# Kernel optimization log

Hardware: AMD Instinct MI355X
Metric: run time of the kernel (lower is better)

Reference implementation:

```python
import jax, jax.numpy as jnp
import numpy as np

K = 100  # sliding-window size hard-coded in the original forward


def setup_inputs() -> dict:
    key = jax.random.key(0)
    x = jax.random.normal(key, (32, 1, 1124, 1124), dtype=jnp.float32)
    return {"x": x}


def reference(x):
    # Sliding 100x100 mean over every stride-1 patch (gq == patch mean),
    # computed via a 2D integral image (summed-area table) so we never
    # materialize the [B, C, outH, outW, K, K] patch tensor.
    B, C, H, W = x.shape
    s = jnp.cumsum(jnp.cumsum(x, axis=2), axis=3)
    # pad one zero row/col at the front -> S has shape [B, C, H+1, W+1]
    S = jnp.pad(s, ((0, 0), (0, 0), (1, 0), (1, 0)))
    sums = (S[:, :, K:, K:] - S[:, :, :-K, K:]
            - S[:, :, K:, :-K] + S[:, :, :-K, :-K])  # [B, C, H-K+1, W-K+1]
    # gq averages over the whole patch (all channels + spatial) -> 1 channel out
    out = jnp.sum(sums, axis=1, keepdims=True) / jnp.asarray(K * K * C, x.dtype)
    return out  # [B, 1, H-99, W-99]
```

## Files before the change

kernel.cpp:

```cpp
#include <hip/hip_runtime.h>


#define H_IN    1124
#define W_IN    1124
#define KWIN    100
#define W_OUT   1025
#define H_OUT   1025
#define TSTR    1032
#define NBANDS  13
#define BANDR   79

typedef float    f32x4 __attribute__((ext_vector_type(4)));
typedef _Float16 f16x4 __attribute__((ext_vector_type(4)));

struct alignas(8) h4 { _Float16 a, b, c, d; };

__global__ __launch_bounds__(256) void hslide_kernel(
    const float* __restrict__ x,
    _Float16* __restrict__ T)
{
    __shared__ float srow[W_IN];
    __shared__ float ps[284];
    __shared__ float qs[280];

    const int row = blockIdx.x;
    const int tid = threadIdx.x;
    const f32x4* xr4 = (const f32x4*)(x + (size_t)row * W_IN);

    for (int i = tid; i < 281; i += 256)
        ((f32x4*)srow)[i] = __builtin_nontemporal_load(xr4 + i);
    __syncthreads();

    f32x4 lo = ((const f32x4*)srow)[tid];
    const float myps = lo[0] + lo[1] + lo[2] + lo[3];
    ps[tid] = myps;
    float myps2 = 0.f;
    if (tid < 25) {
        f32x4 v = ((const f32x4*)srow)[256 + tid];
        myps2 = v[0] + v[1] + v[2] + v[3];
        ps[256 + tid] = myps2;
    }
    __syncthreads();

    qs[tid] = myps + ps[tid + 1] + ps[tid + 2] + ps[tid + 3];
    if (tid < 22)
        qs[256 + tid] = myps2 + ps[257 + tid] + ps[258 + tid] + ps[259 + tid];
    __syncthreads();

    _Float16* trow = T + (size_t)row * TSTR;
    {
        float s = ps[tid + 24];
        #pragma unroll
        for (int i = 0; i < 6; ++i) s += qs[tid + 4 * i];
        f32x4 hi = ((const f32x4*)srow)[tid + 25];
        float s1 = s  + hi[0] - lo[0];
        float s2 = s1 + hi[1] - lo[1];
        float s3 = s2 + hi[2] - lo[2];
        *(h4*)(trow + 4 * tid) = h4{ (_Float16)s, (_Float16)s1,
                                     (_Float16)s2, (_Float16)s3 };
        if (tid == 255) {
            float t = ps[280];
            #pragma unroll
            for (int i = 0; i < 6; ++i) t += qs[256 + 4 * i];
            *(h4*)(trow + 1024) = h4{ (_Float16)t, (_Float16)0.f,
                                      (_Float16)0.f, (_Float16)0.f };
            *(h4*)(trow + 1028) = h4{ (_Float16)0.f, (_Float16)0.f,
                                      (_Float16)0.f, (_Float16)0.f };
        }
    }
}

__global__ __launch_bounds__(256) void vslide_kernel(
    const _Float16* __restrict__ T,
    float* __restrict__ out)
{
    const int tid  = threadIdx.x;
    const int band = blockIdx.x;
    const int b    = blockIdx.y;
    const int r0   = band * BANDR;
    const int nr   = min(BANDR, H_OUT - r0);
    if (nr <= 0) return;

    const int w0 = tid * 4;
    const bool xtra = (tid == 255);
    const float scale = 1.0f / (float)(KWIN * KWIN);

    const _Float16* base = T + ((size_t)b * H_IN + r0) * TSTR + w0;

    float s0 = 0.f, s1 = 0.f, s2 = 0.f, s3 = 0.f, s8 = 0.f;

    {
        const _Float16* p = base;
        for (int cg = 0; cg < 12; ++cg) {
            f16x4 v[8];
            #pragma unroll
            for (int j = 0; j < 8; ++j)
                v[j] = *(const f16x4*)(p + (size_t)j * TSTR);
            #pragma unroll
            for (int j = 0; j < 8; ++j) {
                s0 += (float)v[j][0]; s1 += (float)v[j][1];
                s2 += (float)v[j][2]; s3 += (float)v[j][3];
            }
            if (xtra) {
                #pragma unroll
                for (int j = 0; j < 8; ++j)
                    s8 += (float)*(p + (size_t)j * TSTR + 4);
            }
            p += (size_t)8 * TSTR;
        }
        #pragma unroll
        for (int j = 0; j < 4; ++j) {
            f16x4 v = *(const f16x4*)(p + (size_t)j * TSTR);
            s0 += (float)v[0]; s1 += (float)v[1];
            s2 += (float)v[2]; s3 += (float)v[3];
            if (xtra) s8 += (float)*(p + (size_t)j * TSTR + 4);
        }
    }

    float* q = out + ((size_t)b * H_OUT + r0) * W_OUT + w0;
    __builtin_nontemporal_store(s0 * scale, q + 0);
    __builtin_nontemporal_store(s1 * scale, q + 1);
    __builtin_nontemporal_store(s2 * scale, q + 2);
    __builtin_nontemporal_store(s3 * scale, q + 3);
    if (xtra) __builtin_nontemporal_store(s8 * scale, q + 4);
    q += W_OUT;

    const _Float16* pa = base + (size_t)KWIN * TSTR;
    const _Float16* pd = base;
    const int steps = nr - 1;
    int i = 0;
    for (; i + 8 <= steps; i += 8) {
        f16x4 a[8], d[8];
        #pragma unroll
        for (int j = 0; j < 8; ++j) {
            a[j] = *(const f16x4*)(pa + (size_t)j * TSTR);
            d[j] = *(const f16x4*)(pd + (size_t)j * TSTR);
        }
        #pragma unroll
        for (int j = 0; j < 8; ++j) {
            s0 += (float)a[j][0] - (float)d[j][0];
            s1 += (float)a[j][1] - (float)d[j][1];
            s2 += (float)a[j][2] - (float)d[j][2];
            s3 += (float)a[j][3] - (float)d[j][3];
            __builtin_nontemporal_store(s0 * scale, q + 0);
            __builtin_nontemporal_store(s1 * scale, q + 1);
            __builtin_nontemporal_store(s2 * scale, q + 2);
            __builtin_nontemporal_store(s3 * scale, q + 3);
            if (xtra) {
                s8 += (float)*(pa + (size_t)j * TSTR + 4)
                    - (float)*(pd + (size_t)j * TSTR + 4);
                __builtin_nontemporal_store(s8 * scale, q + 4);
            }
            q += W_OUT;
        }
        pa += (size_t)8 * TSTR;
        pd += (size_t)8 * TSTR;
    }
    for (; i < steps; ++i) {
        f16x4 a = *(const f16x4*)pa, d = *(const f16x4*)pd;
        s0 += (float)a[0] - (float)d[0];
        s1 += (float)a[1] - (float)d[1];
        s2 += (float)a[2] - (float)d[2];
        s3 += (float)a[3] - (float)d[3];
        __builtin_nontemporal_store(s0 * scale, q + 0);
        __builtin_nontemporal_store(s1 * scale, q + 1);
        __builtin_nontemporal_store(s2 * scale, q + 2);
        __builtin_nontemporal_store(s3 * scale, q + 3);
        if (xtra) {
            s8 += (float)*(pa + 4) - (float)*(pd + 4);
            __builtin_nontemporal_store(s8 * scale, q + 4);
        }
        pa += TSTR; pd += TSTR; q += W_OUT;
    }
}

extern "C" void kernel_launch(void* const* d_in, const int* in_sizes, int n_in,
                              void* d_out, int out_size, void* d_ws, size_t ws_size,
                              hipStream_t stream) {
    const float* x = (const float*)d_in[0];
    float* out     = (float*)d_out;
    _Float16* ws   = (_Float16*)d_ws;

    const int B = 32;
    const size_t perBatchT = (size_t)H_IN * TSTR * sizeof(_Float16);

    int G = (int)(ws_size / perBatchT);
    if (G > B) G = B;
    if (G < 1) G = 1;

    for (int b0 = 0; b0 < B; b0 += G) {
        const int g = (B - b0 < G) ? (B - b0) : G;

        hslide_kernel<<<g * H_IN, 256, 0, stream>>>(
            x + (size_t)b0 * H_IN * W_IN, ws);

        dim3 vgrid(NBANDS, g);
        vslide_kernel<<<vgrid, 256, 0, stream>>>(
            ws, out + (size_t)b0 * H_OUT * W_OUT);
    }
}
```

Baseline: 119.8 us.

## Use shared-memory ring buffer of running sums in vertical slide kernel

Result: slower. 130.3 us (+8.7%).

```diff
diff --git a/kernel.cpp b/kernel.cpp
--- a/kernel.cpp
+++ b/kernel.cpp
@@ -7,8 +7,10 @@
 #define W_OUT   1025
 #define H_OUT   1025
 #define TSTR    1032
-#define NBANDS  13
-#define BANDR   79
+#define NBANDS  6
+#define BANDR   171
+#define RSLOT   100
+#define RW      260
 
 typedef float    f32x4 __attribute__((ext_vector_type(4)));
 typedef _Float16 f16x4 __attribute__((ext_vector_type(4)));
@@ -74,103 +76,65 @@
     const _Float16* __restrict__ T,
     float* __restrict__ out)
 {
-    const int tid  = threadIdx.x;
-    const int band = blockIdx.x;
-    const int b    = blockIdx.y;
-    const int r0   = band * BANDR;
-    const int nr   = min(BANDR, H_OUT - r0);
+    __shared__ _Float16 ring[RSLOT][RW];
+
+    const int tid   = threadIdx.x;
+    const int strip = blockIdx.x;
+    const int band  = blockIdx.y;
+    const int b     = blockIdx.z;
+    const int r0    = band * BANDR;
+    const int nr    = min(BANDR, H_OUT - r0);
     if (nr <= 0) return;
+    const int nin   = nr + KWIN - 1;
 
-    const int w0 = tid * 4;
-    const bool xtra = (tid == 255);
+    const int col   = strip * 256 + tid;
+    const bool xtra = (strip == 3) && (tid == 255);
     const float scale = 1.0f / (float)(KWIN * KWIN);
 
-    const _Float16* base = T + ((size_t)b * H_IN + r0) * TSTR + w0;
+    const _Float16* p = T + ((size_t)b * H_IN + r0) * TSTR + col;
+    float* qout       = out + ((size_t)b * H_OUT + r0) * W_OUT + col;
 
-    float s0 = 0.f, s1 = 0.f, s2 = 0.f, s3 = 0.f, s8 = 0.f;
+    float s = 0.f, s2 = 0.f;
+    int slot = 0;
+    int rl = 0;
 
-    {
-        const _Float16* p = base;
-        for (int cg = 0; cg < 12; ++cg) {
-            f16x4 v[8];
+    auto step = [&](float vf, float v2f) {
+        s += vf;
+        if (xtra) s2 += v2f;
+        if (rl >= KWIN) {
+            float old = (float)ring[slot][tid];
+            __builtin_nontemporal_store((s - old) * scale, qout);
+            if (xtra) {
+                float old2 = (float)ring[slot][256];
+                __builtin_nontemporal_store((s2 - old2) * scale, qout + 1);
+            }
+            qout += W_OUT;
+        } else if (rl == KWIN - 1) {
+            __builtin_nontemporal_store(s * scale, qout);
+            if (xtra) __builtin_nontemporal_store(s2 * scale, qout + 1);
+            qout += W_OUT;
+        }
+        ring[slot][tid] = (_Float16)s;
+        if (xtra) ring[slot][256] = (_Float16)s2;
+        if (++slot == RSLOT) slot = 0;
+        ++rl;
+    };
+
+    for (; rl + 16 <= nin; ) {
+        _Float16 v[16], v2[16];
+        #pragma unroll
+        for (int j = 0; j < 16; ++j) v[j] = p[(size_t)(rl + j) * TSTR];
+        if (xtra) {
             #pragma unroll
-            for (int j = 0; j < 8; ++j)
-                v[j] = *(const f16x4*)(p + (size_t)j * TSTR);
-            #pragma unroll
-            for (int j = 0; j < 8; ++j) {
-                s0 += (float)v[j][0]; s1 += (float)v[j][1];
-                s2 += (float)v[j][2]; s3 += (float)v[j][3];
-            }
-            if (xtra) {
-                #pragma unroll
-                for (int j = 0; j < 8; ++j)
-                    s8 += (float)*(p + (size_t)j * TSTR + 4);
-            }
-            p += (size_t)8 * TSTR;
+            for (int j = 0; j < 16; ++j) v2[j] = p[(size_t)(rl + j) * TSTR + 1];
         }
         #pragma unroll
-        for (int j = 0; j < 4; ++j) {
-            f16x4 v = *(const f16x4*)(p + (size_t)j * TSTR);
-            s0 += (float)v[0]; s1 += (float)v[1];
-            s2 += (float)v[2]; s3 += (float)v[3];
-            if (xtra) s8 += (float)*(p + (size_t)j * TSTR + 4);
-        }
+        for (int j = 0; j < 16; ++j) step((float)v[j], xtra ? (float)v2[j] : 0.f);
     }
-
-    float* q = out + ((size_t)b * H_OUT + r0) * W_OUT + w0;
-    __builtin_nontemporal_store(s0 * scale, q + 0);
-    __builtin_nontemporal_store(s1 * scale, q + 1);
-    __builtin_nontemporal_store(s2 * scale, q + 2);
-    __builtin_nontemporal_store(s3 * scale, q + 3);
-    if (xtra) __builtin_nontemporal_store(s8 * scale, q + 4);
-    q += W_OUT;
-
-    const _Float16* pa = base + (size_t)KWIN * TSTR;
-    const _Float16* pd = base;
-    const int steps = nr - 1;
-    int i = 0;
-    for (; i + 8 <= steps; i += 8) {
-        f16x4 a[8], d[8];
-        #pragma unroll
-        for (int j = 0; j < 8; ++j) {
-            a[j] = *(const f16x4*)(pa + (size_t)j * TSTR);
-            d[j] = *(const f16x4*)(pd + (size_t)j * TSTR);
-        }
-        #pragma unroll
-        for (int j = 0; j < 8; ++j) {
-            s0 += (float)a[j][0] - (float)d[j][0];
-            s1 += (float)a[j][1] - (float)d[j][1];
-            s2 += (float)a[j][2] - (float)d[j][2];
-            s3 += (float)a[j][3] - (float)d[j][3];
-            __builtin_nontemporal_store(s0 * scale, q + 0);
-            __builtin_nontemporal_store(s1 * scale, q + 1);
-            __builtin_nontemporal_store(s2 * scale, q + 2);
-            __builtin_nontemporal_store(s3 * scale, q + 3);
-            if (xtra) {
-                s8 += (float)*(pa + (size_t)j * TSTR + 4)
-                    - (float)*(pd + (size_t)j * TSTR + 4);
-                __builtin_nontemporal_store(s8 * scale, q + 4);
-            }
-            q += W_OUT;
-        }
-        pa += (size_t)8 * TSTR;
-        pd += (size_t)8 * TSTR;
-    }
-    for (; i < steps; ++i) {
-        f16x4 a = *(const f16x4*)pa, d = *(const f16x4*)pd;
-        s0 += (float)a[0] - (float)d[0];
-        s1 += (float)a[1] - (float)d[1];
-        s2 += (float)a[2] - (float)d[2];
-        s3 += (float)a[3] - (float)d[3];
-        __builtin_nontemporal_store(s0 * scale, q + 0);
-        __builtin_nontemporal_store(s1 * scale, q + 1);
-        __builtin_nontemporal_store(s2 * scale, q + 2);
-        __builtin_nontemporal_store(s3 * scale, q + 3);
-        if (xtra) {
-            s8 += (float)*(pa + 4) - (float)*(pd + 4);
-            __builtin_nontemporal_store(s8 * scale, q + 4);
-        }
-        pa += TSTR; pd += TSTR; q += W_OUT;
+    for (; rl < nin; ) {
+        _Float16 v  = p[(size_t)rl * TSTR];
+        _Float16 v2 = xtra ? p[(size_t)rl * TSTR + 1] : (_Float16)0.f;
+        step((float)v, (float)v2);
     }
 }
 
@@ -194,7 +158,7 @@
         hslide_kernel<<<g * H_IN, 256, 0, stream>>>(
             x + (size_t)b0 * H_IN * W_IN, ws);
 
-        dim3 vgrid(NBANDS, g);
+        dim3 vgrid(4, NBANDS, g);
         vslide_kernel<<<vgrid, 256, 0, stream>>>(
             ws, out + (size_t)b0 * H_OUT * W_OUT);
     }
```

## Tile intermediate row-sum buffer into 128-column strips and rebalance vertical pass

Applied to the files above, without the earlier changes.

Measured after the change: 108.2 us. 9.7% less time.

```diff
diff --git a/kernel.cpp b/kernel.cpp
--- a/kernel.cpp
+++ b/kernel.cpp
@@ -6,26 +6,28 @@
 #define KWIN    100
 #define W_OUT   1025
 #define H_OUT   1025
-#define TSTR    1032
-#define NBANDS  13
-#define BANDR   79
+#define NBANDS  6
+#define BANDR   171
+#define TROW    128
 
 typedef float    f32x4 __attribute__((ext_vector_type(4)));
-typedef _Float16 f16x4 __attribute__((ext_vector_type(4)));
+typedef _Float16 f16x2 __attribute__((ext_vector_type(2)));
 
 struct alignas(8) h4 { _Float16 a, b, c, d; };
 
 __global__ __launch_bounds__(256) void hslide_kernel(
     const float* __restrict__ x,
-    _Float16* __restrict__ T)
+    _Float16* __restrict__ Tt,
+    _Float16* __restrict__ Tc)
 {
     __shared__ float srow[W_IN];
     __shared__ float ps[284];
     __shared__ float qs[280];
 
     const int row = blockIdx.x;
+    const int b   = blockIdx.y;
     const int tid = threadIdx.x;
-    const f32x4* xr4 = (const f32x4*)(x + (size_t)row * W_IN);
+    const f32x4* xr4 = (const f32x4*)(x + ((size_t)b * H_IN + row) * W_IN);
 
     for (int i = tid; i < 281; i += 256)
         ((f32x4*)srow)[i] = __builtin_nontemporal_load(xr4 + i);
@@ -47,7 +49,6 @@
         qs[256 + tid] = myps2 + ps[257 + tid] + ps[258 + tid] + ps[259 + tid];
     __syncthreads();
 
-    _Float16* trow = T + (size_t)row * TSTR;
     {
         float s = ps[tid + 24];
         #pragma unroll
@@ -56,121 +57,128 @@
         float s1 = s  + hi[0] - lo[0];
         float s2 = s1 + hi[1] - lo[1];
         float s3 = s2 + hi[2] - lo[2];
-        *(h4*)(trow + 4 * tid) = h4{ (_Float16)s, (_Float16)s1,
-                                     (_Float16)s2, (_Float16)s3 };
+
+        const int w0   = tid * 4;
+        const int tile = w0 >> 7;
+        const int c    = w0 & 127;
+        _Float16* dst = Tt + (((size_t)b * 8 + tile) * H_IN + row) * TROW + c;
+        *(h4*)dst = h4{ (_Float16)s, (_Float16)s1, (_Float16)s2, (_Float16)s3 };
+
         if (tid == 255) {
             float t = ps[280];
             #pragma unroll
             for (int i = 0; i < 6; ++i) t += qs[256 + 4 * i];
-            *(h4*)(trow + 1024) = h4{ (_Float16)t, (_Float16)0.f,
-                                      (_Float16)0.f, (_Float16)0.f };
-            *(h4*)(trow + 1028) = h4{ (_Float16)0.f, (_Float16)0.f,
-                                      (_Float16)0.f, (_Float16)0.f };
+            Tc[(size_t)b * H_IN + row] = (_Float16)t;
         }
     }
 }
 
-__global__ __launch_bounds__(256) void vslide_kernel(
-    const _Float16* __restrict__ T,
+__global__ __launch_bounds__(128) void vslide_kernel(
+    const _Float16* __restrict__ Tt,
+    const _Float16* __restrict__ Tc,
     float* __restrict__ out)
 {
     const int tid  = threadIdx.x;
-    const int band = blockIdx.x;
-    const int b    = blockIdx.y;
+    const int tp   = blockIdx.x;
+    const int band = blockIdx.y;
+    const int b    = blockIdx.z;
     const int r0   = band * BANDR;
     const int nr   = min(BANDR, H_OUT - r0);
     if (nr <= 0) return;
 
-    const int w0 = tid * 4;
-    const bool xtra = (tid == 255);
+    const int tile = tp * 2 + (tid >> 6);
+    const int cp   = tid & 63;
+    const int gc   = tile * TROW + 2 * cp;
+    const bool xtra = (tp == 3) && (tid == 127);
     const float scale = 1.0f / (float)(KWIN * KWIN);
 
-    const _Float16* base = T + ((size_t)b * H_IN + r0) * TSTR + w0;
-
-    float s0 = 0.f, s1 = 0.f, s2 = 0.f, s3 = 0.f, s8 = 0.f;
+    const _Float16* base  = Tt + (((size_t)b * 8 + tile) * H_IN + r0) * TROW + 2 * cp;
+    const _Float16* basec = Tc + (size_t)b * H_IN + r0;
+
+    float s0 = 0.f, s1 = 0.f, s8 = 0.f;
 
     {
-        const _Float16* p = base;
+        const _Float16* p  = base;
+        const _Float16* pc = basec;
         for (int cg = 0; cg < 12; ++cg) {
-            f16x4 v[8];
+            f16x2 v[8];
             #pragma unroll
             for (int j = 0; j < 8; ++j)
-                v[j] = *(const f16x4*)(p + (size_t)j * TSTR);
+                v[j] = *(const f16x2*)(p + (size_t)j * TROW);
+            _Float16 vc[8];
+            if (xtra) {
+                #pragma unroll
+                for (int j = 0; j < 8; ++j) vc[j] = pc[j];
+            }
             #pragma unroll
             for (int j = 0; j < 8; ++j) {
                 s0 += (float)v[j][0]; s1 += (float)v[j][1];
-                s2 += (float)v[j][2]; s3 += (float)v[j][3];
             }
             if (xtra) {
                 #pragma unroll
-                for (int j = 0; j < 8; ++j)
-                    s8 += (float)*(p + (size_t)j * TSTR + 4);
-            }
-            p += (size_t)8 * TSTR;
+                for (int j = 0; j < 8; ++j) s8 += (float)vc[j];
+            }
+            p += (size_t)8 * TROW; pc += 8;
         }
         #pragma unroll
         for (int j = 0; j < 4; ++j) {
-            f16x4 v = *(const f16x4*)(p + (size_t)j * TSTR);
+            f16x2 v = *(const f16x2*)(p + (size_t)j * TROW);
             s0 += (float)v[0]; s1 += (float)v[1];
-            s2 += (float)v[2]; s3 += (float)v[3];
-            if (xtra) s8 += (float)*(p + (size_t)j * TSTR + 4);
-        }
-    }
-
-    float* q = out + ((size_t)b * H_OUT + r0) * W_OUT + w0;
+            if (xtra) s8 += (float)pc[j];
+        }
+    }
+
+    float* q = out + ((size_t)b * H_OUT + r0) * W_OUT + gc;
     __builtin_nontemporal_store(s0 * scale, q + 0);
     __builtin_nontemporal_store(s1 * scale, q + 1);
-    __builtin_nontemporal_store(s2 * scale, q + 2);
-    __builtin_nontemporal_store(s3 * scale, q + 3);
-    if (xtra) __builtin_nontemporal_store(s8 * scale, q + 4);
+    if (xtra) __builtin_nontemporal_store(s8 * scale, q + 2);
     q += W_OUT;
 
-    const _Float16* pa = base + (size_t)KWIN * TSTR;
-    const _Float16* pd = base;
+    const _Float16* pa  = base  + (size_t)KWIN * TROW;
+    const _Float16* pd  = base;
+    const _Float16* pac = basec + KWIN;
+    const _Float16* pdc = basec;
     const int steps = nr - 1;
     int i = 0;
     for (; i + 8 <= steps; i += 8) {
-        f16x4 a[8], d[8];
+        f16x2 a[8], d[8];
         #pragma unroll
         for (int j = 0; j < 8; ++j) {
-            a[j] = *(const f16x4*)(pa + (size_t)j * TSTR);
-            d[j] = *(const f16x4*)(pd + (size_t)j * TSTR);
+            a[j] = *(const f16x2*)(pa + (size_t)j * TROW);
+            d[j] = *(const f16x2*)(pd + (size_t)j * TROW);
+        }
+        _Float16 ac[8], dc[8];
+        if (xtra) {
+            #pragma unroll
+            for (int j = 0; j < 8; ++j) { ac[j] = pac[j]; dc[j] = pdc[j]; }
         }
         #pragma unroll
         for (int j = 0; j < 8; ++j) {
             s0 += (float)a[j][0] - (float)d[j][0];
             s1 += (float)a[j][1] - (float)d[j][1];
-            s2 += (float)a[j][2] - (float)d[j][2];
-            s3 += (float)a[j][3] - (float)d[j][3];
             __builtin_nontemporal_store(s0 * scale, q + 0);
             __builtin_nontemporal_store(s1 * scale, q + 1);
-            __builtin_nontemporal_store(s2 * scale, q + 2);
-            __builtin_nontemporal_store(s3 * scale, q + 3);
             if (xtra) {
-                s8 += (float)*(pa + (size_t)j * TSTR + 4)
-                    - (float)*(pd + (size_t)j * TSTR + 4);
-                __builtin_nontemporal_store(s8 * scale, q + 4);
+                s8 += (float)ac[j] - (float)dc[j];
+                __builtin_nontemporal_store(s8 * scale, q + 2);
             }
             q += W_OUT;
         }
-        pa += (size_t)8 * TSTR;
-        pd += (size_t)8 * TSTR;
+        pa += (size_t)8 * TROW; pd += (size_t)8 * TROW;
+        pac += 8; pdc += 8;
     }
     for (; i < steps; ++i) {
-        f16x4 a = *(const f16x4*)pa, d = *(const f16x4*)pd;
+        f16x2 a = *(const f16x2*)pa, d = *(const f16x2*)pd;
         s0 += (float)a[0] - (float)d[0];
         s1 += (float)a[1] - (float)d[1];
-        s2 += (float)a[2] - (float)d[2];
-        s3 += (float)a[3] - (float)d[3];
         __builtin_nontemporal_store(s0 * scale, q + 0);
         __builtin_nontemporal_store(s1 * scale, q + 1);
-        __builtin_nontemporal_store(s2 * scale, q + 2);
-        __builtin_nontemporal_store(s3 * scale, q + 3);
         if (xtra) {
-            s8 += (float)*(pa + 4) - (float)*(pd + 4);
-            __builtin_nontemporal_store(s8 * scale, q + 4);
-        }
-        pa += TSTR; pd += TSTR; q += W_OUT;
+            s8 += (float)*pac - (float)*pdc;
+            ++pac; ++pdc;
+            __builtin_nontemporal_store(s8 * scale, q + 2);
+        }
+        pa += TROW; pd += TROW; q += W_OUT;
     }
 }
 
@@ -182,20 +190,23 @@
     _Float16* ws   = (_Float16*)d_ws;
 
     const int B = 32;
-    const size_t perBatchT = (size_t)H_IN * TSTR * sizeof(_Float16);
-
-    int G = (int)(ws_size / perBatchT);
+    const size_t perBatchH = (size_t)8 * H_IN * TROW + H_IN;
+    int G = (int)(ws_size / (perBatchH * sizeof(_Float16)));
     if (G > B) G = B;
     if (G < 1) G = 1;
 
+    _Float16* Tt = ws;
+    _Float16* Tc = ws + (size_t)G * 8 * H_IN * TROW;
+
     for (int b0 = 0; b0 < B; b0 += G) {
         const int g = (B - b0 < G) ? (B - b0) : G;
 
-        hslide_kernel<<<g * H_IN, 256, 0, stream>>>(
-            x + (size_t)b0 * H_IN * W_IN, ws);
-
-        dim3 vgrid(NBANDS, g);
-        vslide_kernel<<<vgrid, 256, 0, stream>>>(
-            ws, out + (size_t)b0 * H_OUT * W_OUT);
+        dim3 hgrid(H_IN, g);
+        hslide_kernel<<<hgrid, 256, 0, stream>>>(
+            x + (size_t)b0 * H_IN * W_IN, Tt, Tc);
+
+        dim3 vgrid(4, NBANDS, g);
+        vslide_kernel<<<vgrid, 128, 0, stream>>>(
+            Tt, Tc, out + (size_t)b0 * H_OUT * W_OUT);
     }
 }
```
